# Performance work log

Hardware: AMD Instinct MI355X
Metric: run time of the kernel (lower is better)

Reference implementation:

```python
import jax, jax.numpy as jnp
import numpy as np

N_NODES = 100000
N_EDGES = 1600000
D = 128
BETA = 0.001
EPS = 1e-12  # F.normalize eps


def setup_inputs() -> dict:
    key = jax.random.key(0)
    k1, k2, k3, k4, k5, k6 = jax.random.split(key, 6)
    stdv = 1.0 / np.sqrt(D)
    return {
        "input": jax.random.normal(k1, (N_NODES, D), dtype=jnp.float32),
        "edge_rows": jax.random.randint(k2, (N_EDGES,), 0, N_NODES, dtype=jnp.int32),
        "edge_cols": jax.random.randint(k3, (N_EDGES,), 0, N_NODES, dtype=jnp.int32),
        "edge_vals": jax.random.uniform(k4, (N_EDGES,), dtype=jnp.float32),
        "weight": jax.random.uniform(k5, (D, D), minval=-stdv, maxval=stdv, dtype=jnp.float32),
        "bias": jax.random.uniform(k6, (D,), minval=-stdv, maxval=stdv, dtype=jnp.float32),
    }


def reference(input, edge_rows, edge_cols, edge_vals, weight, bias):
    # dense projection: [N, D]
    support = input @ weight
    # sparse neighbor aggregation: agg[i] = sum_{(i,j) in E} adj_val * support[j]
    msgs = edge_vals[:, None] * support[edge_cols]          # [E, D]
    agg = jax.ops.segment_sum(msgs, edge_rows, num_segments=input.shape[0])
    # beta-weighted residual blend
    out = BETA * input + (1.0 - BETA) * agg
    # row-wise L2 normalize (torch F.normalize, p=2, dim=1)
    norm = jnp.sqrt(jnp.sum(out * out, axis=1, keepdims=True))
    out = out / jnp.maximum(norm, EPS)
    # bias add
    return out + bias
```

## Files before the change

### kernel.cpp

```cpp
#include <hip/hip_runtime.h>

#define N_NODES 100000
#define N_EDGES 1600000
#define D 128
#define NB 1563
#define NSUB 8
#define SUBCAP 224
#define CAP (NSUB*SUBCAP)
#define EPT 8
#define SC_BLOCKS 782

typedef short bf16x8 __attribute__((ext_vector_type(8)));
typedef float f32x4 __attribute__((ext_vector_type(4)));

__device__ __forceinline__ unsigned short f2bf(float x){
  union { float f; unsigned u; } v; v.f = x;
  unsigned r = v.u + 0x7fffu + ((v.u >> 16) & 1u);
  return (unsigned short)(r >> 16);
}

__device__ __forceinline__ float bf2f(unsigned short h){
  union { unsigned u; float f; } v; v.u = ((unsigned)h) << 16;
  return v.f;
}

__global__ __launch_bounds__(256) void convert_scatter(
    const float4* __restrict__ in4, ushort4* __restrict__ outb,
    const float* __restrict__ W, unsigned short* __restrict__ WT,
    const int4* __restrict__ rows4, const int4* __restrict__ cols4,
    const float4* __restrict__ vals4,
    int* __restrict__ cursor, int2* __restrict__ edges_s){
  int blk = blockIdx.x;
  if (blk < SC_BLOCKS){
    int tid = blk*256 + threadIdx.x;
    int base = tid * EPT;
    int s = blk & (NSUB-1);
    if (base + EPT <= N_EDGES){
      int4 r0 = rows4[tid*2+0], r1 = rows4[tid*2+1];
      int4 c0 = cols4[tid*2+0], c1 = cols4[tid*2+1];
      float4 v0 = vals4[tid*2+0], v1 = vals4[tid*2+1];
      int r[EPT] = {r0.x, r0.y, r0.z, r0.w, r1.x, r1.y, r1.z, r1.w};
      int c[EPT] = {c0.x, c0.y, c0.z, c0.w, c1.x, c1.y, c1.z, c1.w};
      float v[EPT] = {v0.x, v0.y, v0.z, v0.w, v1.x, v1.y, v1.z, v1.w};
      int pos[EPT];
      #pragma unroll
      for (int k = 0; k < EPT; ++k){
        int b = r[k] >> 6;
        pos[k] = atomicAdd(&cursor[s*NB + b], 1);
      }
      #pragma unroll
      for (int k = 0; k < EPT; ++k){
        int b = r[k] >> 6;
        if (pos[k] < SUBCAP)
          edges_s[(size_t)b*CAP + s*SUBCAP + pos[k]] =
              make_int2(c[k] | ((r[k] & 63) << 17), __float_as_int(v[k]));
      }
    } else {
      const int* rows = (const int*)rows4;
      const int* cols = (const int*)cols4;
      const float* vals = (const float*)vals4;
      for (int k = 0; k < EPT; ++k){
        int i = base + k;
        if (i >= N_EDGES) break;
        int r = rows[i];
        int b = r >> 6;
        int pos = atomicAdd(&cursor[s*NB + b], 1);
        if (pos < SUBCAP)
          edges_s[(size_t)b*CAP + s*SUBCAP + pos] =
              make_int2(cols[i] | ((r & 63) << 17), __float_as_int(vals[i]));
      }
    }
  } else {
    int cb = blk - SC_BLOCKS;
    int i = cb*256 + threadIdx.x;
    if (i < D*D){
      int k = i >> 7, c = i & 127;
      WT[c*128 + k] = f2bf(W[i]);
    }
    float4 a = in4[i];
    ushort4 h;
    h.x = f2bf(a.x); h.y = f2bf(a.y); h.z = f2bf(a.z); h.w = f2bf(a.w);
    outb[i] = h;
  }
}

__global__ __launch_bounds__(512) void agg_final(const ushort4* __restrict__ inb4,
                                                 const int* __restrict__ cursor,
                                                 const int2* __restrict__ edges_g,
                                                 const unsigned short* __restrict__ WTg,
                                                 const float* __restrict__ bias,
                                                 float* __restrict__ out){
  __shared__ unsigned short As[64*136];
  __shared__ int hist[64];
  __shared__ int cur[64];
  __shared__ int rs[64];
  __shared__ int rc[64];
  int2* st = (int2*)As;

  int t = threadIdx.x;
  int b = blockIdx.x;
  size_t base = (size_t)b * CAP;

  if (t < 64) hist[t] = 0;
  __syncthreads();

  int2 held[NSUB];
  int hv = 0;
  #pragma unroll
  for (int s = 0; s < NSUB; ++s){
    int ms = cursor[s*NB + b];
    if (ms > SUBCAP) ms = SUBCAP;
    if (t < ms){
      int2 e = edges_g[base + s*SUBCAP + t];
      held[s] = e;
      hv |= (1 << s);
      atomicAdd(&hist[((unsigned)e.x) >> 17], 1);
    }
  }
  __syncthreads();

  if (t < 64){
    int c = hist[t];
    int x = c;
    #pragma unroll
    for (int o = 1; o < 64; o <<= 1){
      int y = __shfl_up(x, o);
      if (t >= o) x += y;
    }
    int excl = x - c;
    cur[t] = excl;
    rs[t] = excl;
    rc[t] = c;
  }
  __syncthreads();

  #pragma unroll
  for (int s = 0; s < NSUB; ++s){
    if (hv & (1 << s)){
      int2 e = held[s];
      int r = ((unsigned)e.x) >> 17;
      int pos = atomicAdd(&cur[r], 1);
      st[pos] = make_int2(e.x & 0x1FFFF, e.y);
    }
  }
  __syncthreads();

  int grp = t >> 5, l = t & 31;
  float4 res[4];
  #pragma unroll
  for (int j = 0; j < 4; ++j){
    int r = grp*4 + j;
    int e = rs[r], end = e + rc[r];
    float4 a0 = make_float4(0.f,0.f,0.f,0.f);
    float4 a1 = make_float4(0.f,0.f,0.f,0.f);
    float4 a2 = make_float4(0.f,0.f,0.f,0.f);
    float4 a3 = make_float4(0.f,0.f,0.f,0.f);
    for (; e + 4 <= end; e += 4){
      int2 e0 = st[e+0];
      int2 e1 = st[e+1];
      int2 e2 = st[e+2];
      int2 e3 = st[e+3];
      ushort4 x0 = inb4[(size_t)e0.x*32 + l];
      ushort4 x1 = inb4[(size_t)e1.x*32 + l];
      ushort4 x2 = inb4[(size_t)e2.x*32 + l];
      ushort4 x3 = inb4[(size_t)e3.x*32 + l];
      float v0 = __int_as_float(e0.y), v1 = __int_as_float(e1.y);
      float v2 = __int_as_float(e2.y), v3 = __int_as_float(e3.y);
      a0.x = fmaf(v0, bf2f(x0.x), a0.x); a0.y = fmaf(v0, bf2f(x0.y), a0.y);
      a0.z = fmaf(v0, bf2f(x0.z), a0.z); a0.w = fmaf(v0, bf2f(x0.w), a0.w);
      a1.x = fmaf(v1, bf2f(x1.x), a1.x); a1.y = fmaf(v1, bf2f(x1.y), a1.y);
      a1.z = fmaf(v1, bf2f(x1.z), a1.z); a1.w = fmaf(v1, bf2f(x1.w), a1.w);
      a2.x = fmaf(v2, bf2f(x2.x), a2.x); a2.y = fmaf(v2, bf2f(x2.y), a2.y);
      a2.z = fmaf(v2, bf2f(x2.z), a2.z); a2.w = fmaf(v2, bf2f(x2.w), a2.w);
      a3.x = fmaf(v3, bf2f(x3.x), a3.x); a3.y = fmaf(v3, bf2f(x3.y), a3.y);
      a3.z = fmaf(v3, bf2f(x3.z), a3.z); a3.w = fmaf(v3, bf2f(x3.w), a3.w);
    }
    for (; e < end; ++e){
      int2 ee = st[e];
      ushort4 x = inb4[(size_t)ee.x*32 + l];
      float v = __int_as_float(ee.y);
      a0.x = fmaf(v, bf2f(x.x), a0.x); a0.y = fmaf(v, bf2f(x.y), a0.y);
      a0.z = fmaf(v, bf2f(x.z), a0.z); a0.w = fmaf(v, bf2f(x.w), a0.w);
    }
    res[j].x = (a0.x + a1.x) + (a2.x + a3.x);
    res[j].y = (a0.y + a1.y) + (a2.y + a3.y);
    res[j].z = (a0.z + a1.z) + (a2.z + a3.z);
    res[j].w = (a0.w + a1.w) + (a2.w + a3.w);
  }
  __syncthreads();

  #pragma unroll
  for (int j = 0; j < 4; ++j){
    int r = grp*4 + j;
    ushort4 h;
    h.x = f2bf(res[j].x); h.y = f2bf(res[j].y);
    h.z = f2bf(res[j].z); h.w = f2bf(res[j].w);
    *((ushort4*)&As[r*136 + l*4]) = h;
  }
  __syncthreads();

  int wave = t >> 6, lane = t & 63;
  int q = lane >> 4, n = lane & 15;
  bf16x8 afr[4];
  if (t < 256){
    #pragma unroll
    for (int ks = 0; ks < 4; ++ks)
      afr[ks] = *((const bf16x8*)&As[(wave*16 + n)*136 + ks*32 + q*8]);
  }
  __syncthreads();

  int block_row = b * 64;
  #pragma unroll
  for (int i = 0; i < 4; ++i){
    int idx4 = i*512 + t;
    int row = idx4 >> 5, k4 = idx4 & 31;
    int grow = block_row + row;
    ushort4 h = make_ushort4(0,0,0,0);
    if (grow < N_NODES) h = inb4[(size_t)grow*32 + k4];
    *((ushort4*)&As[row*136 + k4*4]) = h;
  }
  __syncthreads();
  if (t >= 256) return;

  f32x4 acc[8];
  #pragma unroll
  for (int ct = 0; ct < 8; ++ct) acc[ct] = (f32x4){0.f, 0.f, 0.f, 0.f};

  #pragma unroll
  for (int ct = 0; ct < 8; ++ct){
    #pragma unroll
    for (int ks = 0; ks < 4; ++ks){
      bf16x8 bfr = *((const bf16x8*)(WTg + (ct*16 + n)*128 + ks*32 + q*8));
      acc[ct] = __builtin_amdgcn_mfma_f32_16x16x32_bf16(afr[ks], bfr, acc[ct], 0, 0, 0);
    }
  }

  int base_row = block_row + wave*16 + q*4;
  float v[8][4];
  float s[4] = {0.f, 0.f, 0.f, 0.f};
  #pragma unroll
  for (int reg = 0; reg < 4; ++reg){
    int row_local = wave*16 + q*4 + reg;
    #pragma unroll
    for (int ct = 0; ct < 8; ++ct){
      float inp = bf2f(As[row_local*136 + ct*16 + n]);
      float val = fmaf(0.999f, acc[ct][reg], 0.001f * inp);
      v[ct][reg] = val;
      s[reg] = fmaf(val, val, s[reg]);
    }
  }
  #pragma unroll
  for (int reg = 0; reg < 4; ++reg){
    float x = s[reg];
    x += __shfl_xor(x, 1);
    x += __shfl_xor(x, 2);
    x += __shfl_xor(x, 4);
    x += __shfl_xor(x, 8);
    s[reg] = x;
  }
  #pragma unroll
  for (int reg = 0; reg < 4; ++reg){
    int grow = base_row + reg;
    if (grow >= N_NODES) continue;
    float scale = 1.f / fmaxf(sqrtf(s[reg]), 1e-12f);
    float* outrow = out + (size_t)grow * D;
    #pragma unroll
    for (int ct = 0; ct < 8; ++ct){
      outrow[ct*16 + n] = fmaf(v[ct][reg], scale, bias[ct*16 + n]);
    }
  }
}

extern "C" void kernel_launch(void* const* d_in, const int* in_sizes, int n_in,
                              void* d_out, int out_size, void* d_ws, size_t ws_size,
                              hipStream_t stream){
  const float* input  = (const float*)d_in[0];
  const int*   erows  = (const int*)d_in[1];
  const int*   ecols  = (const int*)d_in[2];
  const float* evals  = (const float*)d_in[3];
  const float* weight = (const float*)d_in[4];
  const float* bias   = (const float*)d_in[5];
  float* out = (float*)d_out;

  int*   cursor    = (int*)d_ws;
  int2*  edges_s   = (int2*)(cursor + NSUB*NB);
  ushort4* inb     = (ushort4*)(edges_s + (size_t)NB*CAP);
  unsigned short* WTg = (unsigned short*)(inb + (size_t)N_NODES * 32);

  hipMemsetAsync(cursor, 0, NSUB * NB * sizeof(int), stream);
  convert_scatter<<<SC_BLOCKS + 12500, 256, 0, stream>>>(
      (const float4*)input, inb, weight, WTg,
      (const int4*)erows, (const int4*)ecols, (const float4*)evals,
      cursor, edges_s);
  agg_final<<<NB, 512, 0, stream>>>((const ushort4*)inb, cursor, edges_s,
                                    WTg, bias, out);
}
```

Baseline: 318.3 us.

## Pad bucket cursors, split convert/scatter kernels, use all 8 waves for MFMA epilogue

Pads each atomic cursor to its own 64-byte slot so bucket counters stop sharing cache lines under contention. Splits the fused convert+scatter launch into two separate kernels. In agg_final, all 8 waves now do the GEMM and epilogue, each covering half the output columns, with row norms combined through shared memory. This trades an extra launch, a larger memset and an extra barrier for less atomic contention and twice the active waves in the tail.

After: 299.7 us. -5.8%, faster.

```diff
diff --git a/kernel.cpp b/kernel.cpp
--- a/kernel.cpp
+++ b/kernel.cpp
@@ -9,6 +9,7 @@
 #define CAP (NSUB*SUBCAP)
 #define EPT 8
 #define SC_BLOCKS 782
+#define CSTRIDE 16
 
 typedef short bf16x8 __attribute__((ext_vector_type(8)));
 typedef float f32x4 __attribute__((ext_vector_type(4)));
@@ -24,63 +25,63 @@
   return v.f;
 }
 
-__global__ __launch_bounds__(256) void convert_scatter(
-    const float4* __restrict__ in4, ushort4* __restrict__ outb,
-    const float* __restrict__ W, unsigned short* __restrict__ WT,
-    const int4* __restrict__ rows4, const int4* __restrict__ cols4,
-    const float4* __restrict__ vals4,
-    int* __restrict__ cursor, int2* __restrict__ edges_s){
-  int blk = blockIdx.x;
-  if (blk < SC_BLOCKS){
-    int tid = blk*256 + threadIdx.x;
-    int base = tid * EPT;
-    int s = blk & (NSUB-1);
-    if (base + EPT <= N_EDGES){
-      int4 r0 = rows4[tid*2+0], r1 = rows4[tid*2+1];
-      int4 c0 = cols4[tid*2+0], c1 = cols4[tid*2+1];
-      float4 v0 = vals4[tid*2+0], v1 = vals4[tid*2+1];
-      int r[EPT] = {r0.x, r0.y, r0.z, r0.w, r1.x, r1.y, r1.z, r1.w};
-      int c[EPT] = {c0.x, c0.y, c0.z, c0.w, c1.x, c1.y, c1.z, c1.w};
-      float v[EPT] = {v0.x, v0.y, v0.z, v0.w, v1.x, v1.y, v1.z, v1.w};
-      int pos[EPT];
-      #pragma unroll
-      for (int k = 0; k < EPT; ++k){
-        int b = r[k] >> 6;
-        pos[k] = atomicAdd(&cursor[s*NB + b], 1);
-      }
-      #pragma unroll
-      for (int k = 0; k < EPT; ++k){
-        int b = r[k] >> 6;
-        if (pos[k] < SUBCAP)
-          edges_s[(size_t)b*CAP + s*SUBCAP + pos[k]] =
-              make_int2(c[k] | ((r[k] & 63) << 17), __float_as_int(v[k]));
-      }
-    } else {
-      const int* rows = (const int*)rows4;
-      const int* cols = (const int*)cols4;
-      const float* vals = (const float*)vals4;
-      for (int k = 0; k < EPT; ++k){
-        int i = base + k;
-        if (i >= N_EDGES) break;
-        int r = rows[i];
-        int b = r >> 6;
-        int pos = atomicAdd(&cursor[s*NB + b], 1);
-        if (pos < SUBCAP)
-          edges_s[(size_t)b*CAP + s*SUBCAP + pos] =
-              make_int2(cols[i] | ((r & 63) << 17), __float_as_int(vals[i]));
-      }
+__global__ __launch_bounds__(256) void convert_input(const float4* __restrict__ in4,
+                                                     ushort4* __restrict__ outb,
+                                                     const float* __restrict__ W,
+                                                     unsigned short* __restrict__ WT){
+  int i = blockIdx.x*256 + threadIdx.x;
+  if (i < D*D){
+    int k = i >> 7, c = i & 127;
+    WT[c*128 + k] = f2bf(W[i]);
+  }
+  float4 a = in4[i];
+  ushort4 h;
+  h.x = f2bf(a.x); h.y = f2bf(a.y); h.z = f2bf(a.z); h.w = f2bf(a.w);
+  outb[i] = h;
+}
+
+__global__ __launch_bounds__(256) void scatter_direct(const int4* __restrict__ rows4,
+                                                      const int4* __restrict__ cols4,
+                                                      const float4* __restrict__ vals4,
+                                                      int* __restrict__ cursor,
+                                                      int2* __restrict__ edges_s){
+  int tid = blockIdx.x*256 + threadIdx.x;
+  int base = tid * EPT;
+  int s = blockIdx.x & (NSUB-1);
+  if (base + EPT <= N_EDGES){
+    int4 r0 = rows4[tid*2+0], r1 = rows4[tid*2+1];
+    int4 c0 = cols4[tid*2+0], c1 = cols4[tid*2+1];
+    float4 v0 = vals4[tid*2+0], v1 = vals4[tid*2+1];
+    int r[EPT] = {r0.x, r0.y, r0.z, r0.w, r1.x, r1.y, r1.z, r1.w};
+    int c[EPT] = {c0.x, c0.y, c0.z, c0.w, c1.x, c1.y, c1.z, c1.w};
+    float v[EPT] = {v0.x, v0.y, v0.z, v0.w, v1.x, v1.y, v1.z, v1.w};
+    int pos[EPT];
+    #pragma unroll
+    for (int k = 0; k < EPT; ++k){
+      int b = r[k] >> 6;
+      pos[k] = atomicAdd(&cursor[(s*NB + b)*CSTRIDE], 1);
+    }
+    #pragma unroll
+    for (int k = 0; k < EPT; ++k){
+      int b = r[k] >> 6;
+      if (pos[k] < SUBCAP)
+        edges_s[(size_t)b*CAP + s*SUBCAP + pos[k]] =
+            make_int2(c[k] | ((r[k] & 63) << 17), __float_as_int(v[k]));
     }
   } else {
-    int cb = blk - SC_BLOCKS;
-    int i = cb*256 + threadIdx.x;
-    if (i < D*D){
-      int k = i >> 7, c = i & 127;
-      WT[c*128 + k] = f2bf(W[i]);
-    }
-    float4 a = in4[i];
-    ushort4 h;
-    h.x = f2bf(a.x); h.y = f2bf(a.y); h.z = f2bf(a.z); h.w = f2bf(a.w);
-    outb[i] = h;
+    const int* rows = (const int*)rows4;
+    const int* cols = (const int*)cols4;
+    const float* vals = (const float*)vals4;
+    for (int k = 0; k < EPT; ++k){
+      int i = base + k;
+      if (i >= N_EDGES) break;
+      int r = rows[i];
+      int b = r >> 6;
+      int pos = atomicAdd(&cursor[(s*NB + b)*CSTRIDE], 1);
+      if (pos < SUBCAP)
+        edges_s[(size_t)b*CAP + s*SUBCAP + pos] =
+            make_int2(cols[i] | ((r & 63) << 17), __float_as_int(vals[i]));
+    }
   }
 }
 
@@ -95,6 +96,7 @@
   __shared__ int cur[64];
   __shared__ int rs[64];
   __shared__ int rc[64];
+  __shared__ float rsum[2][64];
   int2* st = (int2*)As;
 
   int t = threadIdx.x;
@@ -108,7 +110,7 @@
   int hv = 0;
   #pragma unroll
   for (int s = 0; s < NSUB; ++s){
-    int ms = cursor[s*NB + b];
+    int ms = cursor[(s*NB + b)*CSTRIDE];
     if (ms > SUBCAP) ms = SUBCAP;
     if (t < ms){
       int2 e = edges_g[base + s*SUBCAP + t];
@@ -199,14 +201,13 @@
   }
   __syncthreads();
 
-  int wave = t >> 6, lane = t & 63;
+  int w = t >> 6, lane = t & 63;
+  int wr = w >> 1, wc = w & 1;
   int q = lane >> 4, n = lane & 15;
   bf16x8 afr[4];
-  if (t < 256){
-    #pragma unroll
-    for (int ks = 0; ks < 4; ++ks)
-      afr[ks] = *((const bf16x8*)&As[(wave*16 + n)*136 + ks*32 + q*8]);
-  }
+  #pragma unroll
+  for (int ks = 0; ks < 4; ++ks)
+    afr[ks] = *((const bf16x8*)&As[(wr*16 + n)*136 + ks*32 + q*8]);
   __syncthreads();
 
   int block_row = b * 64;
@@ -220,30 +221,28 @@
     *((ushort4*)&As[row*136 + k4*4]) = h;
   }
   __syncthreads();
-  if (t >= 256) return;
-
-  f32x4 acc[8];
-  #pragma unroll
-  for (int ct = 0; ct < 8; ++ct) acc[ct] = (f32x4){0.f, 0.f, 0.f, 0.f};
-
-  #pragma unroll
-  for (int ct = 0; ct < 8; ++ct){
+
+  f32x4 acc[4];
+  #pragma unroll
+  for (int ct = 0; ct < 4; ++ct) acc[ct] = (f32x4){0.f, 0.f, 0.f, 0.f};
+
+  #pragma unroll
+  for (int ct = 0; ct < 4; ++ct){
     #pragma unroll
     for (int ks = 0; ks < 4; ++ks){
-      bf16x8 bfr = *((const bf16x8*)(WTg + (ct*16 + n)*128 + ks*32 + q*8));
+      bf16x8 bfr = *((const bf16x8*)(WTg + (wc*64 + ct*16 + n)*128 + ks*32 + q*8));
       acc[ct] = __builtin_amdgcn_mfma_f32_16x16x32_bf16(afr[ks], bfr, acc[ct], 0, 0, 0);
     }
   }
 
-  int base_row = block_row + wave*16 + q*4;
-  float v[8][4];
+  float v[4][4];
   float s[4] = {0.f, 0.f, 0.f, 0.f};
   #pragma unroll
   for (int reg = 0; reg < 4; ++reg){
-    int row_local = wave*16 + q*4 + reg;
-    #pragma unroll
-    for (int ct = 0; ct < 8; ++ct){
-      float inp = bf2f(As[row_local*136 + ct*16 + n]);
+    int row_local = wr*16 + q*4 + reg;
+    #pragma unroll
+    for (int ct = 0; ct < 4; ++ct){
+      float inp = bf2f(As[row_local*136 + wc*64 + ct*16 + n]);
       float val = fmaf(0.999f, acc[ct][reg], 0.001f * inp);
       v[ct][reg] = val;
       s[reg] = fmaf(val, val, s[reg]);
@@ -258,15 +257,25 @@
     x += __shfl_xor(x, 8);
     s[reg] = x;
   }
+  if (n == 0){
+    #pragma unroll
+    for (int reg = 0; reg < 4; ++reg)
+      rsum[wc][wr*16 + q*4 + reg] = s[reg];
+  }
+  __syncthreads();
+
   #pragma unroll
   for (int reg = 0; reg < 4; ++reg){
-    int grow = base_row + reg;
+    int row_local = wr*16 + q*4 + reg;
+    int grow = block_row + row_local;
     if (grow >= N_NODES) continue;
-    float scale = 1.f / fmaxf(sqrtf(s[reg]), 1e-12f);
+    float tot = rsum[0][row_local] + rsum[1][row_local];
+    float scale = 1.f / fmaxf(sqrtf(tot), 1e-12f);
     float* outrow = out + (size_t)grow * D;
     #pragma unroll
-    for (int ct = 0; ct < 8; ++ct){
-      outrow[ct*16 + n] = fmaf(v[ct][reg], scale, bias[ct*16 + n]);
+    for (int ct = 0; ct < 4; ++ct){
+      int c = wc*64 + ct*16 + n;
+      outrow[c] = fmaf(v[ct][reg], scale, bias[c]);
     }
   }
 }
@@ -283,15 +292,14 @@
   float* out = (float*)d_out;
 
   int*   cursor    = (int*)d_ws;
-  int2*  edges_s   = (int2*)(cursor + NSUB*NB);
+  int2*  edges_s   = (int2*)(cursor + NSUB*NB*CSTRIDE);
   ushort4* inb     = (ushort4*)(edges_s + (size_t)NB*CAP);
   unsigned short* WTg = (unsigned short*)(inb + (size_t)N_NODES * 32);
 
-  hipMemsetAsync(cursor, 0, NSUB * NB * sizeof(int), stream);
-  convert_scatter<<<SC_BLOCKS + 12500, 256, 0, stream>>>(
-      (const float4*)input, inb, weight, WTg,
-      (const int4*)erows, (const int4*)ecols, (const float4*)evals,
-      cursor, edges_s);
+  hipMemsetAsync(cursor, 0, (size_t)NSUB * NB * CSTRIDE * sizeof(int), stream);
+  convert_input<<<12500, 256, 0, stream>>>((const float4*)input, inb, weight, WTg);
+  scatter_direct<<<SC_BLOCKS, 256, 0, stream>>>((const int4*)erows, (const int4*)ecols,
+                                                (const float4*)evals, cursor, edges_s);
   agg_final<<<NB, 512, 0, stream>>>((const ushort4*)inb, cursor, edges_s,
                                     WTg, bias, out);
 }
```
